# Kernel tuning notes

Hardware: AMD Instinct MI355X
Metric: run time of the kernel (lower is better)

Reference implementation:

```python
import jax, jax.numpy as jnp
import numpy as np

N_NODES = 100000
N_EDGES = 1600000
IN_DIM = 256
OUT_DIM = 128


def setup_inputs() -> dict:
    key = jax.random.key(0)
    k1, k2, k3, k4, k5 = jax.random.split(key, 5)
    inputs = jax.random.normal(k1, (N_NODES, IN_DIM), dtype=jnp.float32)
    # xavier_uniform with relu gain, as in the torch init
    gain = float(np.sqrt(2.0))
    limit = gain * float(np.sqrt(6.0 / (IN_DIM + OUT_DIM)))
    W = jax.random.uniform(k2, (IN_DIM, OUT_DIM), dtype=jnp.float32,
                           minval=-limit, maxval=limit)
    edge_src = jax.random.randint(k3, (N_EDGES,), 0, N_NODES, dtype=jnp.int32)
    edge_dst = jax.random.randint(k4, (N_EDGES,), 0, N_NODES, dtype=jnp.int32)
    edge_val = jax.random.uniform(k5, (N_EDGES,), dtype=jnp.float32)
    return {"inputs": inputs, "W": W, "edge_src": edge_src,
            "edge_dst": edge_dst, "edge_val": edge_val}


def reference(inputs, W, edge_src, edge_dst, edge_val):
    # x = inputs @ W  (dense GEMM)
    h = inputs @ W                                  # [N, OUT_DIM]
    # adj @ h  as SpMM over COO edges: out[d] += val * h[s]
    msg = edge_val[:, None] * h[edge_src]           # [E, OUT_DIM]
    agg = jax.ops.segment_sum(msg, edge_dst, num_segments=N_NODES)
    # act = ReLU, fused with SpMM output
    return jax.nn.relu(agg)
```

## Files before the change

### kernel.cpp

```cpp
#include <hip/hip_runtime.h>
#include <hip/hip_bf16.h>

#define N_NODES 100000
#define N_EDGES 1600000
#define IN_DIM  256
#define OUT_DIM 128

#define GEMM_ROWS   32
#define GEMM_BLOCKS (N_NODES / GEMM_ROWS)

#define NBUCK   196
#define BSHIFT  9
#define BCAP    10240
#define BSTRIDE 16
#define EPB     2048
#define BIN_BLOCKS ((N_EDGES + EPB - 1) / EPB)
#define TOTAL_BLOCKS (GEMM_BLOCKS + BIN_BLOCKS)

typedef __attribute__((ext_vector_type(8))) short bf16x8;
typedef __attribute__((ext_vector_type(4))) float f32x4;

__device__ __forceinline__ ushort f2bf(float f) {
    union { float f; unsigned u; } v; v.f = f;
    unsigned r = v.u + 0x7FFF + ((v.u >> 16) & 1);
    return (ushort)(r >> 16);
}
__device__ __forceinline__ float bflo(unsigned u) {
    union { unsigned u; float f; } v; v.u = u << 16; return v.f;
}
__device__ __forceinline__ float bfhi(unsigned u) {
    union { unsigned u; float f; } v; v.u = u & 0xFFFF0000u; return v.f;
}

__global__ __launch_bounds__(256) void pack_w(const float* __restrict__ W,
                                              ushort* __restrict__ Wp,
                                              int* __restrict__ bcur) {
    const int t = blockIdx.x * 256 + threadIdx.x;
    if (blockIdx.x == 0) {
        for (int i = threadIdx.x; i < NBUCK * BSTRIDE; i += 256) bcur[i] = 0;
    }
    if (t >= 4096) return;
    const int kk = t >> 9, n = (t >> 6) & 7, l = t & 63;
    const int kbase = kk * 32 + (l >> 4) * 8;
    const int col   = n * 16 + (l & 15);
    ushort* o = Wp + (size_t)t * 8;
#pragma unroll
    for (int j = 0; j < 8; ++j)
        o[j] = f2bf(W[(size_t)(kbase + j) * OUT_DIM + col]);
}

__global__ __launch_bounds__(256, 5) void gemm_coarse(const float* __restrict__ X,
                                                      const bf16x8* __restrict__ Bp,
                                                      ushort* __restrict__ H,
                                                      const int* __restrict__ esrc,
                                                      const int* __restrict__ edst,
                                                      const float* __restrict__ eval,
                                                      int* __restrict__ bcur,
                                                      int2* __restrict__ binned) {
    __shared__ char smem[22656];

    const int tid  = threadIdx.x;
    const int lane = tid & 63;
    const int wv   = tid >> 6;
    const int bid  = blockIdx.x;

    const bool is_coarse = ((bid % 5) == 4) || (bid == TOTAL_BLOCKS - 1);

    if (is_coarse) {
        const int blk = (bid == TOTAL_BLOCKS - 1) ? (BIN_BLOCKS - 1) : (bid / 5);
        int*   cnt   = (int*)smem;
        int*   lbase = (int*)smem + 256;
        int*   sbase = (int*)smem + 512;
        int*   cur   = (int*)smem + 768;
        int2*  lrec  = (int2*)(smem + 4096);
        unsigned char* lbid = (unsigned char*)smem + 20480;

        const int cb  = blk * EPB;
        const int lim = (N_EDGES - cb < EPB) ? (N_EDGES - cb) : EPB;

        if (tid < NBUCK) cnt[tid] = 0;
        __syncthreads();
        for (int i = tid; i < lim; i += 256)
            atomicAdd(&cnt[edst[cb + i] >> BSHIFT], 1);
        __syncthreads();

        {
            __shared__ int wsum[4];
            const int v = (tid < NBUCK) ? cnt[tid] : 0;
            int sv = v;
#pragma unroll
            for (int d = 1; d < 64; d <<= 1) {
                const int t = __shfl_up(sv, d, 64);
                if (lane >= d) sv += t;
            }
            if (lane == 63) wsum[wv] = sv;
            __syncthreads();
            int wx = 0;
#pragma unroll
            for (int w = 0; w < 4; ++w) if (w < wv) wx += wsum[w];
            if (tid < NBUCK) {
                const int ex = wx + sv - v;
                lbase[tid] = ex;
                cur[tid]   = ex;
                sbase[tid] = v ? atomicAdd(&bcur[tid * BSTRIDE], v) : 0;
            }
        }
        __syncthreads();

        for (int i = tid; i < lim; i += 256) {
            const int d = edst[cb + i];
            const int b = d >> BSHIFT;
            const int pos = atomicAdd(&cur[b], 1);
            int2 rec;
            rec.x = esrc[cb + i] | ((d & 511) << 20);
            rec.y = __float_as_int(eval[cb + i]);
            lrec[pos] = rec;
            lbid[pos] = (unsigned char)b;
        }
        __syncthreads();

        for (int i = tid; i < lim; i += 256) {
            const int b   = lbid[i];
            const int off = sbase[b] + (i - lbase[b]);
            if (off < BCAP)
                binned[(size_t)b * BCAP + off] = lrec[i];
        }
        return;
    }

    const int gidx = bid - bid / 5;
    ushort* xt = (ushort*)smem;
    const int row0 = gidx * GEMM_ROWS;
    const int wid  = wv;

#pragma unroll 4
    for (int it = 0; it < 8; ++it) {
        const int tr = it * 4 + (tid >> 6);
        const int tc = (tid & 63) * 4;
        const float4 v = *reinterpret_cast<const float4*>(
            X + (size_t)(row0 + tr) * IN_DIM + tc);
        ushort4 b4;
        b4.x = f2bf(v.x); b4.y = f2bf(v.y); b4.z = f2bf(v.z); b4.w = f2bf(v.w);
        const int byte = (tr * 512 + tc * 2) ^ ((tr & 7) << 4);
        *reinterpret_cast<ushort4*>((char*)xt + byte) = b4;
    }

    bf16x8 Bfr[8][2];
#pragma unroll
    for (int kk = 0; kk < 8; ++kk)
#pragma unroll
        for (int n = 0; n < 2; ++n)
            Bfr[kk][n] = Bp[(size_t)(kk * 8 + wid * 2 + n) * 64 + lane];

    __syncthreads();

    const int rlo  = lane & 15;
    const int kseg = lane >> 4;
    const int rl0  = rlo;
    const int rl1  = rlo + 16;
    const int rxor = (rlo & 7) << 4;

    f32x4 acc[2][2] = {};

#pragma unroll
    for (int kk = 0; kk < 8; ++kk) {
        const int cb2 = (kk * 64 + kseg * 16) ^ rxor;
        const bf16x8 A0 = *reinterpret_cast<const bf16x8*>((const char*)xt + rl0 * 512 + cb2);
        const bf16x8 A1 = *reinterpret_cast<const bf16x8*>((const char*)xt + rl1 * 512 + cb2);
#pragma unroll
        for (int n = 0; n < 2; ++n) {
            acc[0][n] = __builtin_amdgcn_mfma_f32_16x16x32_bf16(A0, Bfr[kk][n], acc[0][n], 0, 0, 0);
            acc[1][n] = __builtin_amdgcn_mfma_f32_16x16x32_bf16(A1, Bfr[kk][n], acc[1][n], 0, 0, 0);
        }
    }

#pragma unroll
    for (int i = 0; i < 2; ++i)
#pragma unroll
        for (int r = 0; r < 4; ++r)
#pragma unroll
            for (int n = 0; n < 2; ++n)
                H[(size_t)(row0 + i * 16 + kseg * 4 + r) * OUT_DIM
                  + wid * 32 + n * 16 + rlo] = f2bf(acc[i][n][r]);
}

__global__ __launch_bounds__(1024) void bin_pull(const int* __restrict__ bcur,
                                                 const int2* __restrict__ binned,
                                                 const ushort* __restrict__ H,
                                                 float* __restrict__ out) {
    __shared__ int2 srec[BCAP];
    __shared__ int nh[512];
    __shared__ int cur[512];
    __shared__ int ws[4];
    const int b   = blockIdx.x;
    const int tid = threadIdx.x, lane = tid & 63, wid = tid >> 6;
    const int node0 = b << BSHIFT;
    int nn = N_NODES - node0; if (nn > 512) nn = 512;
    int size = bcur[b * BSTRIDE]; if (size > BCAP) size = BCAP;
    const int2* in = binned + (size_t)b * BCAP;

    if (tid < 512) nh[tid] = 0;
    __syncthreads();
    for (int k = tid; k < size; k += 1024)
        atomicAdd(&nh[(in[k].x >> 20) & 511], 1);
    __syncthreads();

    int a0 = 0, ts = 0, sv = 0;
    if (tid < 256) {
        a0 = nh[2 * tid];
        const int a1 = nh[2 * tid + 1];
        ts = a0 + a1;
        sv = ts;
#pragma unroll
        for (int d = 1; d < 64; d <<= 1) {
            const int t = __shfl_up(sv, d, 64);
            if (lane >= d) sv += t;
        }
        if (lane == 63) ws[wid] = sv;
    }
    __syncthreads();
    if (tid < 256) {
        int wx = 0;
#pragma unroll
        for (int w = 0; w < 4; ++w) if (w < wid) wx += ws[w];
        const int ex = wx + sv - ts;
        cur[2 * tid]     = ex;
        cur[2 * tid + 1] = ex + a0;
    }
    __syncthreads();

    for (int k = tid; k < size; k += 1024) {
        const int2 r = in[k];
        const int pos = atomicAdd(&cur[(r.x >> 20) & 511], 1);
        int2 o; o.x = r.x & 0xFFFFF; o.y = r.y;
        srec[pos] = o;
    }
    __syncthreads();

    const int grp = tid >> 4;
    const int c   = tid & 15;

#define ACC(h, v)  {                                                      \
        p0 = fmaf(v, bflo(h.x), p0);  p1 = fmaf(v, bfhi(h.x), p1);        \
        p2 = fmaf(v, bflo(h.y), p2);  p3 = fmaf(v, bfhi(h.y), p3);        \
        p4 = fmaf(v, bflo(h.z), p4);  p5 = fmaf(v, bfhi(h.z), p5);        \
        p6 = fmaf(v, bflo(h.w), p6);  p7 = fmaf(v, bfhi(h.w), p7); }

    for (int j = 0; j < 8; ++j) {
        const int ln = grp * 8 + j;
        if (ln >= nn) break;
        const int end = cur[ln];
        const int beg = end - nh[ln];

        float p0 = 0.f, p1 = 0.f, p2 = 0.f, p3 = 0.f;
        float p4 = 0.f, p5 = 0.f, p6 = 0.f, p7 = 0.f;

        int e = beg;
        for (; e + 7 < end; e += 8) {
            const int2 r0 = srec[e + 0], r1 = srec[e + 1];
            const int2 r2 = srec[e + 2], r3 = srec[e + 3];
            const int2 r4 = srec[e + 4], r5 = srec[e + 5];
            const int2 r6 = srec[e + 6], r7 = srec[e + 7];
            const uint4 h0 = *((const uint4*)(H + (size_t)r0.x * OUT_DIM) + c);
            const uint4 h1 = *((const uint4*)(H + (size_t)r1.x * OUT_DIM) + c);
            const uint4 h2 = *((const uint4*)(H + (size_t)r2.x * OUT_DIM) + c);
            const uint4 h3 = *((const uint4*)(H + (size_t)r3.x * OUT_DIM) + c);
            const uint4 h4 = *((const uint4*)(H + (size_t)r4.x * OUT_DIM) + c);
            const uint4 h5 = *((const uint4*)(H + (size_t)r5.x * OUT_DIM) + c);
            const uint4 h6 = *((const uint4*)(H + (size_t)r6.x * OUT_DIM) + c);
            const uint4 h7 = *((const uint4*)(H + (size_t)r7.x * OUT_DIM) + c);
            ACC(h0, __int_as_float(r0.y));  ACC(h1, __int_as_float(r1.y));
            ACC(h2, __int_as_float(r2.y));  ACC(h3, __int_as_float(r3.y));
            ACC(h4, __int_as_float(r4.y));  ACC(h5, __int_as_float(r5.y));
            ACC(h6, __int_as_float(r6.y));  ACC(h7, __int_as_float(r7.y));
        }
        for (; e + 1 < end; e += 2) {
            const int2 r0 = srec[e + 0], r1 = srec[e + 1];
            const uint4 h0 = *((const uint4*)(H + (size_t)r0.x * OUT_DIM) + c);
            const uint4 h1 = *((const uint4*)(H + (size_t)r1.x * OUT_DIM) + c);
            ACC(h0, __int_as_float(r0.y));  ACC(h1, __int_as_float(r1.y));
        }
        if (e < end) {
            const int2 r0 = srec[e];
            const uint4 h0 = *((const uint4*)(H + (size_t)r0.x * OUT_DIM) + c);
            ACC(h0, __int_as_float(r0.y));
        }

        float* op = out + (size_t)(node0 + ln) * OUT_DIM + c * 8;
        float4 o0, o1;
        o0.x = fmaxf(p0, 0.f); o0.y = fmaxf(p1, 0.f);
        o0.z = fmaxf(p2, 0.f); o0.w = fmaxf(p3, 0.f);
        o1.x = fmaxf(p4, 0.f); o1.y = fmaxf(p5, 0.f);
        o1.z = fmaxf(p6, 0.f); o1.w = fmaxf(p7, 0.f);
        *reinterpret_cast<float4*>(op)     = o0;
        *reinterpret_cast<float4*>(op + 4) = o1;
    }
#undef ACC
}

extern "C" void kernel_launch(void* const* d_in, const int* in_sizes, int n_in,
                              void* d_out, int out_size, void* d_ws, size_t ws_size,
                              hipStream_t stream) {
    const float* X    = (const float*)d_in[0];
    const float* W    = (const float*)d_in[1];
    const int*   esrc = (const int*)d_in[2];
    const int*   edst = (const int*)d_in[3];
    const float* eval = (const float*)d_in[4];
    float*       out  = (float*)d_out;

    char* ws = (char*)d_ws;
    ushort* Hb     = (ushort*)ws;  ws += (size_t)N_NODES * OUT_DIM * sizeof(ushort);
    ushort* Wp     = (ushort*)ws;  ws += (size_t)4096 * 8 * sizeof(ushort);
    int*    bcur   = (int*)ws;     ws += (size_t)NBUCK * BSTRIDE * 4;
    int2*   binned = (int2*)ws;

    pack_w<<<16, 256, 0, stream>>>(W, Wp, bcur);
    gemm_coarse<<<TOTAL_BLOCKS, 256, 0, stream>>>(X, (const bf16x8*)Wp, Hb,
                                                  esrc, edst, eval, bcur, binned);

    bin_pull<<<NBUCK, 1024, 0, stream>>>(bcur, binned, Hb, out);
}
```

Baseline: 108.7 us.

## Split each bucket's pull across two blocks of 256 nodes each

The pull kernel now launches two blocks per bucket, and each block handles half of the 512 destination nodes. Each block reads the whole bucket's records but counts and scatters only those for its half, so it needs half the shared memory for records and counters. The aim is more blocks on a 256-CU GPU (392 instead of 196) and better occupancy. The cost is that every bucket's records are read twice from global memory. The guarded write also silently drops records if one half overflows 5120.

```diff
diff --git a/kernel.cpp b/kernel.cpp
--- a/kernel.cpp
+++ b/kernel.cpp
@@ -12,6 +12,7 @@
 #define NBUCK   196
 #define BSHIFT  9
 #define BCAP    10240
+#define BCAP_H  5120
 #define BSTRIDE 16
 #define EPB     2048
 #define BIN_BLOCKS ((N_EDGES + EPB - 1) / EPB)
@@ -188,29 +189,31 @@
                                                  const int2* __restrict__ binned,
                                                  const ushort* __restrict__ H,
                                                  float* __restrict__ out) {
-    __shared__ int2 srec[BCAP];
-    __shared__ int nh[512];
-    __shared__ int cur[512];
+    __shared__ int2 srec[BCAP_H];
+    __shared__ int nh[256];
+    __shared__ int cur[256];
     __shared__ int ws[4];
-    const int b   = blockIdx.x;
+    const int b    = blockIdx.x >> 1;
+    const int half = blockIdx.x & 1;
     const int tid = threadIdx.x, lane = tid & 63, wid = tid >> 6;
-    const int node0 = b << BSHIFT;
-    int nn = N_NODES - node0; if (nn > 512) nn = 512;
+    const int node0 = (b << BSHIFT) + half * 256;
+    int nn = N_NODES - node0; if (nn > 256) nn = 256;
+    if (nn <= 0) return;
     int size = bcur[b * BSTRIDE]; if (size > BCAP) size = BCAP;
     const int2* in = binned + (size_t)b * BCAP;
 
-    if (tid < 512) nh[tid] = 0;
-    __syncthreads();
-    for (int k = tid; k < size; k += 1024)
-        atomicAdd(&nh[(in[k].x >> 20) & 511], 1);
-    __syncthreads();
-
-    int a0 = 0, ts = 0, sv = 0;
+    if (tid < 256) nh[tid] = 0;
+    __syncthreads();
+    for (int k = tid; k < size; k += 1024) {
+        const int ln9 = (in[k].x >> 20) & 511;
+        if ((ln9 >> 8) == half) atomicAdd(&nh[ln9 & 255], 1);
+    }
+    __syncthreads();
+
+    int v = 0, sv = 0;
     if (tid < 256) {
-        a0 = nh[2 * tid];
-        const int a1 = nh[2 * tid + 1];
-        ts = a0 + a1;
-        sv = ts;
+        v = nh[tid];
+        sv = v;
 #pragma unroll
         for (int d = 1; d < 64; d <<= 1) {
             const int t = __shfl_up(sv, d, 64);
@@ -223,17 +226,19 @@
         int wx = 0;
 #pragma unroll
         for (int w = 0; w < 4; ++w) if (w < wid) wx += ws[w];
-        const int ex = wx + sv - ts;
-        cur[2 * tid]     = ex;
-        cur[2 * tid + 1] = ex + a0;
+        cur[tid] = wx + sv - v;
     }
     __syncthreads();
 
     for (int k = tid; k < size; k += 1024) {
         const int2 r = in[k];
-        const int pos = atomicAdd(&cur[(r.x >> 20) & 511], 1);
-        int2 o; o.x = r.x & 0xFFFFF; o.y = r.y;
-        srec[pos] = o;
+        const int ln9 = (r.x >> 20) & 511;
+        if ((ln9 >> 8) != half) continue;
+        const int pos = atomicAdd(&cur[ln9 & 255], 1);
+        if (pos < BCAP_H) {
+            int2 o; o.x = r.x & 0xFFFFF; o.y = r.y;
+            srec[pos] = o;
+        }
     }
     __syncthreads();
 
@@ -246,8 +251,8 @@
         p4 = fmaf(v, bflo(h.z), p4);  p5 = fmaf(v, bfhi(h.z), p5);        \
         p6 = fmaf(v, bflo(h.w), p6);  p7 = fmaf(v, bfhi(h.w), p7); }
 
-    for (int j = 0; j < 8; ++j) {
-        const int ln = grp * 8 + j;
+    for (int j = 0; j < 4; ++j) {
+        const int ln = grp * 4 + j;
         if (ln >= nn) break;
         const int end = cur[ln];
         const int beg = end - nh[ln];
@@ -318,5 +323,5 @@
     gemm_coarse<<<TOTAL_BLOCKS, 256, 0, stream>>>(X, (const bf16x8*)Wp, Hb,
                                                   esrc, edst, eval, bcur, binned);
 
-    bin_pull<<<NBUCK, 1024, 0, stream>>>(bcur, binned, Hb, out);
-}
+    bin_pull<<<2 * NBUCK, 1024, 0, stream>>>(bcur, binned, Hb, out);
+}
```

Result: slower. 113.2 us (+4.1%).
